# Performance work log

Measured on AMD Instinct MI355X. Metric: run time of the kernel, lower is better.

Reference implementation:

```python
import jax, jax.numpy as jnp
import numpy as np

N_NODES = 50000
N_HEDGES = 100000
N_INC = 600000
F_IN = 512
HID = 128
EPS = 1e-5
ALPHA = 0.5


def layer_norm(x, g, b):
    mu = jnp.mean(x, axis=-1, keepdims=True)
    var = jnp.mean((x - mu) ** 2, axis=-1, keepdims=True)
    return (x - mu) * jax.lax.rsqrt(var + EPS) * g + b


def scatter_mean(src, idx, num_segments):
    s = jax.ops.segment_sum(src, idx, num_segments=num_segments)
    c = jax.ops.segment_sum(jnp.ones((src.shape[0], 1), src.dtype), idx, num_segments=num_segments)
    return jnp.where(c > 0, s / jnp.maximum(c, 1.0), 0.0)


def setup_inputs() -> dict:
    key = jax.random.key(0)
    ks = jax.random.split(key, 20)

    def lin(k, fi, fo):
        kw, kb = jax.random.split(k)
        w = jax.random.normal(kw, (fi, fo), jnp.float32) / np.sqrt(fi)
        b = jax.random.normal(kb, (fo,), jnp.float32) * 0.01
        return w, b

    x1 = jax.random.normal(ks[0], (N_NODES, F_IN), jnp.float32)
    x2 = jax.random.normal(ks[1], (N_NODES, F_IN), jnp.float32)
    v1 = jax.random.randint(ks[2], (N_INC,), 0, N_NODES, jnp.int32)
    e1 = jax.random.randint(ks[3], (N_INC,), 0, N_HEDGES, jnp.int32)
    v2 = jax.random.randint(ks[4], (N_INC,), 0, N_NODES, jnp.int32)
    e2 = jax.random.randint(ks[5], (N_INC,), 0, N_HEDGES, jnp.int32)

    lin_w, lin_b = lin(ks[6], F_IN, HID)
    w1_w, w1_b = lin(ks[7], HID, HID)
    w2_w, w2_b = lin(ks[8], 2 * HID, HID)
    w_w, w_b = lin(ks[9], HID, HID)
    cls_w1, cls_b1 = lin(ks[10], HID, 64)
    cls_w2, cls_b2 = lin(ks[11], 64, 1)

    return {
        "x1": x1, "v1": v1, "e1": e1, "x2": x2, "v2": v2, "e2": e2,
        "lin_w": lin_w, "lin_b": lin_b,
        "w1_ln_g": jnp.ones((HID,)), "w1_ln_b": jnp.zeros((HID,)), "w1_w": w1_w, "w1_b": w1_b,
        "w2_ln_g": jnp.ones((2 * HID,)), "w2_ln_b": jnp.zeros((2 * HID,)), "w2_w": w2_w, "w2_b": w2_b,
        "w_ln_g": jnp.ones((HID,)), "w_ln_b": jnp.zeros((HID,)), "w_w": w_w, "w_b": w_b,
        "cls_w1": cls_w1, "cls_b1": cls_b1,
        "cls_ln_g": jnp.ones((64,)), "cls_ln_b": jnp.zeros((64,)),
        "cls_w2": cls_w2, "cls_b2": cls_b2,
    }


def _conv(X, v, e, X0, p):
    # W1 (LN + Linear) on vertices, gather to incidence pairs
    Xve = (layer_norm(X, p["w1_ln_g"], p["w1_ln_b"]) @ p["w1_w"] + p["w1_b"])[v]  # [E, H]
    Xe = scatter_mean(Xve, e, N_HEDGES)                                             # [M, H]
    Xev = Xe[e]                                                                      # [E, H]
    cat = jnp.concatenate([X[v], Xev], axis=-1)                                      # [E, 2H]
    Xev = layer_norm(cat, p["w2_ln_g"], p["w2_ln_b"]) @ p["w2_w"] + p["w2_b"]      # [E, H]
    Xv = scatter_mean(Xev, v, X.shape[0])                                            # [N, H]
    X = (1.0 - ALPHA) * Xv + ALPHA * X0
    return layer_norm(X, p["w_ln_g"], p["w_ln_b"]) @ p["w_w"] + p["w_b"]


def _branch(x, v, e, p):
    x = jax.nn.relu(x @ p["lin_w"] + p["lin_b"])
    x0 = x
    for _ in range(2):  # nlayer=2, shared conv weights
        x = jax.nn.relu(_conv(x, v, e, x0, p))
    # classifier MLP: Linear -> relu -> LN -> Linear
    h = jax.nn.relu(x @ p["cls_w1"] + p["cls_b1"])
    h = layer_norm(h, p["cls_ln_g"], p["cls_ln_b"])
    return h @ p["cls_w2"] + p["cls_b2"]


def reference(x1, v1, e1, x2, v2, e2,
              lin_w, lin_b,
              w1_ln_g, w1_ln_b, w1_w, w1_b,
              w2_ln_g, w2_ln_b, w2_w, w2_b,
              w_ln_g, w_ln_b, w_w, w_b,
              cls_w1, cls_b1, cls_ln_g, cls_ln_b, cls_w2, cls_b2):
    p = dict(lin_w=lin_w, lin_b=lin_b,
             w1_ln_g=w1_ln_g, w1_ln_b=w1_ln_b, w1_w=w1_w, w1_b=w1_b,
             w2_ln_g=w2_ln_g, w2_ln_b=w2_ln_b, w2_w=w2_w, w2_b=w2_b,
             w_ln_g=w_ln_g, w_ln_b=w_ln_b, w_w=w_w, w_b=w_b,
             cls_w1=cls_w1, cls_b1=cls_b1, cls_ln_g=cls_ln_g, cls_ln_b=cls_ln_b,
             cls_w2=cls_w2, cls_b2=cls_b2)
    return (_branch(x1, v1, e1, p), _branch(x2, v2, e2, p))
```

## Files before the change

kernel.cpp:

```cpp
#include <hip/hip_runtime.h>

#define NN 50000
#define NH 100000
#define NI 600000
#define FIN 512
#define HID 128
#define LNEPS 1e-5f

static __device__ __forceinline__ void fma4(float4& a, float s, const float4& w) {
  a.x += s * w.x; a.y += s * w.y; a.z += s * w.z; a.w += s * w.w;
}

__global__ void k_hist(const int* __restrict__ idx, int n, int* __restrict__ deg) {
  int i = blockIdx.x * 256 + threadIdx.x;
  if (i < n) atomicAdd(&deg[idx[i]], 1);
}

__global__ __launch_bounds__(1024) void k_scan1(int* __restrict__ data, int m,
                                                int* __restrict__ bsums) {
  __shared__ int sh[1024];
  int tid = threadIdx.x;
  int i = blockIdx.x * 1024 + tid;
  int v = (i < m) ? data[i] : 0;
  sh[tid] = v;
  __syncthreads();
  for (int off = 1; off < 1024; off <<= 1) {
    int tv = (tid >= off) ? sh[tid - off] : 0;
    __syncthreads();
    sh[tid] += tv;
    __syncthreads();
  }
  if (i < m) data[i] = sh[tid] - v;
  if (tid == 1023) bsums[blockIdx.x] = sh[1023];
}

__global__ __launch_bounds__(1024) void k_scan2(int* __restrict__ bsums, int nb) {
  __shared__ int sh[1024];
  int tid = threadIdx.x;
  int v = (tid < nb) ? bsums[tid] : 0;
  sh[tid] = v;
  __syncthreads();
  for (int off = 1; off < 1024; off <<= 1) {
    int tv = (tid >= off) ? sh[tid - off] : 0;
    __syncthreads();
    sh[tid] += tv;
    __syncthreads();
  }
  if (tid < nb) bsums[tid] = sh[tid] - v;
}

__global__ void k_scan3(int* __restrict__ data, const int* __restrict__ bsums,
                        int m, int total) {
  int i = blockIdx.x * 256 + threadIdx.x;
  if (i < m) data[i] += bsums[i >> 10];
  if (i == 0) data[m] = total;
}

__global__ void k_fill(const int* __restrict__ key, const int* __restrict__ oth, int n,
                       const int* __restrict__ starts, int* __restrict__ cursor,
                       int* __restrict__ out_oth) {
  int i = blockIdx.x * 256 + threadIdx.x;
  if (i >= n) return;
  int k = key[i];
  int pos = starts[k] + atomicAdd(&cursor[k], 1);
  out_oth[pos] = oth[i];
}

__global__ void k_sort_seg(const int* __restrict__ starts, int nseg,
                           int* __restrict__ vals) {
  int seg = blockIdx.x * 256 + threadIdx.x;
  if (seg >= nseg) return;
  int s = starts[seg], e = starts[seg + 1];
  int d = e - s;
  if (d <= 1) return;
  if (d <= 48) {
    int buf[48];
    for (int i = 0; i < d; i++) buf[i] = vals[s + i];
    for (int i = 1; i < d; i++) {
      int key = buf[i], j = i - 1;
      while (j >= 0 && buf[j] > key) { buf[j + 1] = buf[j]; j--; }
      buf[j + 1] = key;
    }
    for (int i = 0; i < d; i++) vals[s + i] = buf[i];
  } else {
    for (int i = s + 1; i < e; i++) {
      int key = vals[i], j = i - 1;
      while (j >= s && vals[j] > key) { vals[j + 1] = vals[j]; j--; }
      vals[j + 1] = key;
    }
  }
}

__global__ void k_prep_w2g(const float* __restrict__ W2, const float* __restrict__ g2,
                           float* __restrict__ W2g) {
  int i = blockIdx.x * 256 + threadIdx.x;
  if (i >= 256 * 128) return;
  int k = i >> 7;
  W2g[i] = g2[k] * W2[i];
}

__global__ __launch_bounds__(128) void k_prep_sgc0(
    const float* __restrict__ W2, const float* __restrict__ g2,
    const float* __restrict__ b2, const float* __restrict__ bias2,
    float* __restrict__ s_g, float* __restrict__ c0) {
  int t = threadIdx.x;
  float sg = 0.f, cc = 0.f;
  for (int k = 0; k < 256; k++) {
    float w = W2[k * 128 + t];
    sg += g2[k] * w;
    cc += b2[k] * w;
  }
  s_g[t] = sg;
  c0[t] = cc + bias2[t];
}

static __device__ __forceinline__ void gemm_inner(
    const float (*Ash)[132], const float (*Wsh)[68], int tc, int tr,
    float4& acc0, float4& acc1) {
#pragma unroll 8
  for (int k = 0; k < 128; k += 4) {
    float4 w0 = *(const float4*)&Wsh[k + 0][tc * 4];
    float4 w1 = *(const float4*)&Wsh[k + 1][tc * 4];
    float4 w2 = *(const float4*)&Wsh[k + 2][tc * 4];
    float4 w3 = *(const float4*)&Wsh[k + 3][tc * 4];
    float4 a0 = *(const float4*)&Ash[tr * 2 + 0][k];
    float4 a1 = *(const float4*)&Ash[tr * 2 + 1][k];
    fma4(acc0, a0.x, w0); fma4(acc0, a0.y, w1); fma4(acc0, a0.z, w2); fma4(acc0, a0.w, w3);
    fma4(acc1, a1.x, w0); fma4(acc1, a1.y, w1); fma4(acc1, a1.z, w2); fma4(acc1, a1.w, w3);
  }
}

template <bool BIAS, bool RELU>
static __device__ __forceinline__ void tile_gemm_out(
    const float (*Ash)[132], float (*Wsh)[68], const float* __restrict__ W,
    const float* __restrict__ bias, float* __restrict__ out, int r0, int N, int t) {
  const int tc = t & 15, tr = t >> 4;
  for (int ch = 0; ch < 2; ch++) {
    __syncthreads();
    for (int s = t; s < 2048; s += 256) {
      int k = s >> 4, c4 = (s & 15) * 4;
      *(float4*)&Wsh[k][c4] = *(const float4*)(W + (size_t)k * 128 + ch * 64 + c4);
    }
    __syncthreads();
    float4 acc0 = {0, 0, 0, 0}, acc1 = {0, 0, 0, 0};
    gemm_inner(Ash, (const float(*)[68])Wsh, tc, tr, acc0, acc1);
    int c = ch * 64 + tc * 4;
    float4 bb = {0, 0, 0, 0};
    if (BIAS) bb = *(const float4*)(bias + c);
    int row0 = r0 + tr * 2;
    if (row0 < N) {
      float4 o;
      o.x = acc0.x + bb.x; o.y = acc0.y + bb.y; o.z = acc0.z + bb.z; o.w = acc0.w + bb.w;
      if (RELU) { o.x = fmaxf(o.x, 0.f); o.y = fmaxf(o.y, 0.f); o.z = fmaxf(o.z, 0.f); o.w = fmaxf(o.w, 0.f); }
      *(float4*)(out + (size_t)row0 * 128 + c) = o;
    }
    if (row0 + 1 < N) {
      float4 o;
      o.x = acc1.x + bb.x; o.y = acc1.y + bb.y; o.z = acc1.z + bb.z; o.w = acc1.w + bb.w;
      if (RELU) { o.x = fmaxf(o.x, 0.f); o.y = fmaxf(o.y, 0.f); o.z = fmaxf(o.z, 0.f); o.w = fmaxf(o.w, 0.f); }
      *(float4*)(out + (size_t)(row0 + 1) * 128 + c) = o;
    }
  }
}

template <bool LN, bool BIAS, bool RELU>
__global__ __launch_bounds__(256) void k_tile128(
    const float* __restrict__ A, const float* __restrict__ W,
    const float* __restrict__ bias, const float* __restrict__ lng,
    const float* __restrict__ lnb, float* __restrict__ sn,
    float* __restrict__ qn, float* __restrict__ out, int N) {
  __shared__ float Ash[32][132];
  __shared__ float Wsh[128][68];
  const int t = threadIdx.x;
  const int r0 = blockIdx.x * 32;
  for (int s = t; s < 1024; s += 256) {
    int r = s >> 5, c4 = (s & 31) * 4;
    float4 val = {0, 0, 0, 0};
    if (r0 + r < N) val = *(const float4*)(A + (size_t)(r0 + r) * 128 + c4);
    *(float4*)&Ash[r][c4] = val;
  }
  if (LN) {
    __syncthreads();
    int wv = t >> 6, lane = t & 63;
    for (int j = 0; j < 8; j++) {
      int r = wv * 8 + j;
      if (r0 + r < N) {
        float2 x = *(float2*)&Ash[r][lane * 2];
        float s = x.x + x.y, sq = x.x * x.x + x.y * x.y;
        for (int m = 1; m < 64; m <<= 1) { s += __shfl_xor(s, m); sq += __shfl_xor(sq, m); }
        if (lane == 0) { sn[r0 + r] = s; qn[r0 + r] = sq; }
        float mu = s * (1.f / 128.f);
        float var = sq * (1.f / 128.f) - mu * mu;
        float rstd = rsqrtf(var + LNEPS);
        float2 gg = ((const float2*)lng)[lane];
        float2 bb = ((const float2*)lnb)[lane];
        float2 o;
        o.x = (x.x - mu) * rstd * gg.x + bb.x;
        o.y = (x.y - mu) * rstd * gg.y + bb.y;
        *(float2*)&Ash[r][lane * 2] = o;
      }
    }
  }
  tile_gemm_out<BIAS, RELU>((const float(*)[132])Ash, Wsh, W, bias, out, r0, N, t);
}

__global__ __launch_bounds__(256) void k_proj(
    const float* __restrict__ A, const float* __restrict__ W,
    const float* __restrict__ bias, float* __restrict__ out,
    float* __restrict__ out2, int N) {
  __shared__ float Ash[32][132];
  __shared__ float Wsh[128][68];
  const int t = threadIdx.x;
  const int r0 = blockIdx.x * 32;
  const int tc = t & 15, tr = t >> 4;
  for (int ch = 0; ch < 2; ch++) {
    float4 acc0 = {0, 0, 0, 0}, acc1 = {0, 0, 0, 0};
    for (int kc = 0; kc < 4; kc++) {
      __syncthreads();
      for (int s = t; s < 1024; s += 256) {
        int r = s >> 5, c4 = (s & 31) * 4;
        float4 val = {0, 0, 0, 0};
        if (r0 + r < N) val = *(const float4*)(A + (size_t)(r0 + r) * 512 + kc * 128 + c4);
        *(float4*)&Ash[r][c4] = val;
      }
      for (int s = t; s < 2048; s += 256) {
        int k = s >> 4, c4 = (s & 15) * 4;
        *(float4*)&Wsh[k][c4] = *(const float4*)(W + (size_t)(kc * 128 + k) * 128 + ch * 64 + c4);
      }
      __syncthreads();
      gemm_inner((const float(*)[132])Ash, (const float(*)[68])Wsh, tc, tr, acc0, acc1);
    }
    int c = ch * 64 + tc * 4;
    float4 bb = *(const float4*)(bias + c);
    int row0 = r0 + tr * 2;
    if (row0 < N) {
      float4 o;
      o.x = fmaxf(acc0.x + bb.x, 0.f); o.y = fmaxf(acc0.y + bb.y, 0.f);
      o.z = fmaxf(acc0.z + bb.z, 0.f); o.w = fmaxf(acc0.w + bb.w, 0.f);
      *(float4*)(out + (size_t)row0 * 128 + c) = o;
      *(float4*)(out2 + (size_t)row0 * 128 + c) = o;
    }
    if (row0 + 1 < N) {
      float4 o;
      o.x = fmaxf(acc1.x + bb.x, 0.f); o.y = fmaxf(acc1.y + bb.y, 0.f);
      o.z = fmaxf(acc1.z + bb.z, 0.f); o.w = fmaxf(acc1.w + bb.w, 0.f);
      *(float4*)(out + (size_t)(row0 + 1) * 128 + c) = o;
      *(float4*)(out2 + (size_t)(row0 + 1) * 128 + c) = o;
    }
  }
}

__global__ __launch_bounds__(256) void k_xe(
    const float* __restrict__ B, const int* __restrict__ starts,
    const int* __restrict__ vlist, float* __restrict__ Xe,
    float* __restrict__ se, float* __restrict__ qe, int M) {
  int half = threadIdx.x >> 5, lane = threadIdx.x & 31;
  int m = blockIdx.x * 8 + half;
  if (m >= M) return;
  int s = starts[m], e = starts[m + 1];
  float4 acc = {0.f, 0.f, 0.f, 0.f};
  for (int j = s; j < e; j++) {
    int vv = vlist[j];
    float4 val = ((const float4*)(B + (size_t)vv * 128))[lane];
    acc.x += val.x; acc.y += val.y; acc.z += val.z; acc.w += val.w;
  }
  int d = e - s;
  float inv = d > 0 ? 1.f / (float)d : 0.f;
  float4 o = {acc.x * inv, acc.y * inv, acc.z * inv, acc.w * inv};
  ((float4*)(Xe + (size_t)m * 128))[lane] = o;
  float ss = o.x + o.y + o.z + o.w;
  float qq = o.x * o.x + o.y * o.y + o.z * o.z + o.w * o.w;
  for (int mm = 1; mm < 32; mm <<= 1) {
    ss += __shfl_xor(ss, mm, 32);
    qq += __shfl_xor(qq, mm, 32);
  }
  if (lane == 0) { se[m] = ss; qe[m] = qq; }
}

__global__ __launch_bounds__(256) void k_nodeg(
    const float* __restrict__ X, const float* __restrict__ Xe,
    const int* __restrict__ starts_v, const int* __restrict__ e_by_v,
    const float* __restrict__ sn, const float* __restrict__ qn,
    const float* __restrict__ se, const float* __restrict__ qe,
    float* __restrict__ P, float* __restrict__ Qb,
    float* __restrict__ invdeg, float* __restrict__ t2arr, int N) {
  int half = threadIdx.x >> 5, lane = threadIdx.x & 31;
  int v = blockIdx.x * 8 + half;
  if (v >= N) return;
  int s = starts_v[v], e = starts_v[v + 1];
  float svn = sn[v], qvn = qn[v];
  float4 acc = {0.f, 0.f, 0.f, 0.f};
  float suma = 0.f, sumb = 0.f;
  for (int j = s; j < e; j++) {
    int ee = e_by_v[j];
    float mu = (svn + se[ee]) * (1.f / 256.f);
    float e2 = (qvn + qe[ee]) * (1.f / 256.f);
    float rstd = rsqrtf(e2 - mu * mu + LNEPS);
    suma += rstd;
    sumb += mu * rstd;
    float4 vv = ((const float4*)(Xe + (size_t)ee * 128))[lane];
    acc.x += rstd * vv.x; acc.y += rstd * vv.y;
    acc.z += rstd * vv.z; acc.w += rstd * vv.w;
  }
  float4 xr = ((const float4*)(X + (size_t)v * 128))[lane];
  float4 pp = {suma * xr.x, suma * xr.y, suma * xr.z, suma * xr.w};
  ((float4*)(P + (size_t)v * 128))[lane] = pp;
  ((float4*)(Qb + (size_t)v * 128))[lane] = acc;
  if (lane == 0) {
    int d = e - s;
    float inv = d > 0 ? 1.f / (float)d : 0.f;
    invdeg[v] = inv;
    t2arr[v] = sumb * inv;
  }
}

__global__ __launch_bounds__(256) void k_tile256(
    const float* __restrict__ P, const float* __restrict__ Q,
    const float* __restrict__ W, const float* __restrict__ invdeg,
    const float* __restrict__ t2arr, const float* __restrict__ s_g,
    const float* __restrict__ c0, const float* __restrict__ X0,
    const float* __restrict__ wg, const float* __restrict__ wbn,
    float* __restrict__ out, int N) {
  __shared__ float Ash[32][260];
  __shared__ float Wsh[64][68];
  const int t = threadIdx.x;
  const int r0 = blockIdx.x * 32;
  for (int s = t; s < 2048; s += 256) {
    int r = s >> 6, c4 = (s & 63) * 4;
    float4 val = {0, 0, 0, 0};
    if (r0 + r < N) {
      val = (c4 < 128) ? *(const float4*)(P + (size_t)(r0 + r) * 128 + c4)
                       : *(const float4*)(Q + (size_t)(r0 + r) * 128 + (c4 - 128));
    }
    *(float4*)&Ash[r][c4] = val;
  }
  const int tc = t & 15, tr = t >> 4;
  float4 acc[2][2] = {{{0,0,0,0},{0,0,0,0}},{{0,0,0,0},{0,0,0,0}}};
  for (int ch = 0; ch < 2; ch++) {
    for (int kc = 0; kc < 4; kc++) {
      __syncthreads();
      for (int s = t; s < 1024; s += 256) {
        int k = s >> 4, c4 = (s & 15) * 4;
        *(float4*)&Wsh[k][c4] = *(const float4*)(W + (size_t)(kc * 64 + k) * 128 + ch * 64 + c4);
      }
      __syncthreads();
#pragma unroll 4
      for (int k = 0; k < 64; k += 4) {
        float4 w0 = *(const float4*)&Wsh[k + 0][tc * 4];
        float4 w1 = *(const float4*)&Wsh[k + 1][tc * 4];
        float4 w2 = *(const float4*)&Wsh[k + 2][tc * 4];
        float4 w3 = *(const float4*)&Wsh[k + 3][tc * 4];
        float4 a0 = *(const float4*)&Ash[tr * 2 + 0][kc * 64 + k];
        float4 a1 = *(const float4*)&Ash[tr * 2 + 1][kc * 64 + k];
        fma4(acc[ch][0], a0.x, w0); fma4(acc[ch][0], a0.y, w1);
        fma4(acc[ch][0], a0.z, w2); fma4(acc[ch][0], a0.w, w3);
        fma4(acc[ch][1], a1.x, w0); fma4(acc[ch][1], a1.y, w1);
        fma4(acc[ch][1], a1.z, w2); fma4(acc[ch][1], a1.w, w3);
      }
    }
  }
  __syncthreads();
  for (int r = 0; r < 2; r++) {
    int row = r0 + tr * 2 + r;
    if (row < N) {
      float t1 = invdeg[row], t2 = t2arr[row];
      float flag = t1 > 0.f ? 1.f : 0.f;
      for (int ch = 0; ch < 2; ch++) {
        int c = ch * 64 + tc * 4;
        float4 g = acc[ch][r];
        float4 sg = *(const float4*)(s_g + c);
        float4 cc = *(const float4*)(c0 + c);
        float4 x0 = *(const float4*)(X0 + (size_t)row * 128 + c);
        float4 z;
        z.x = 0.5f * (g.x * t1 - t2 * sg.x + flag * cc.x) + 0.5f * x0.x;
        z.y = 0.5f * (g.y * t1 - t2 * sg.y + flag * cc.y) + 0.5f * x0.y;
        z.z = 0.5f * (g.z * t1 - t2 * sg.z + flag * cc.z) + 0.5f * x0.z;
        z.w = 0.5f * (g.w * t1 - t2 * sg.w + flag * cc.w) + 0.5f * x0.w;
        *(float4*)&Ash[tr * 2 + r][c] = z;
      }
    }
  }
  __syncthreads();
  int wv = t >> 6, lane = t & 63;
  for (int j = 0; j < 8; j++) {
    int r = wv * 8 + j;
    if (r0 + r < N) {
      float2 x = *(float2*)&Ash[r][lane * 2];
      float s = x.x + x.y, sq = x.x * x.x + x.y * x.y;
      for (int m = 1; m < 64; m <<= 1) { s += __shfl_xor(s, m); sq += __shfl_xor(sq, m); }
      float mu = s * (1.f / 128.f);
      float var = sq * (1.f / 128.f) - mu * mu;
      float rstd = rsqrtf(var + LNEPS);
      float2 gg = ((const float2*)wg)[lane];
      float2 bb = ((const float2*)wbn)[lane];
      float2 o;
      o.x = (x.x - mu) * rstd * gg.x + bb.x;
      o.y = (x.y - mu) * rstd * gg.y + bb.y;
      *(float2*)(out + (size_t)(r0 + r) * 128 + lane * 2) = o;
    }
  }
}

__global__ __launch_bounds__(128) void k_cls(
    const float* __restrict__ X, const float* __restrict__ W1,
    const float* __restrict__ b1, const float* __restrict__ lg,
    const float* __restrict__ lb, const float* __restrict__ W2,
    const float* __restrict__ b2, float* __restrict__ out, int N) {
  __shared__ float xr[128];
  int n = blockIdx.x, t = threadIdx.x;
  xr[t] = X[(size_t)n * 128 + t];
  __syncthreads();
  if (t < 64) {
    float a = b1[t];
    for (int k = 0; k < 128; k++) a += xr[k] * W1[k * 64 + t];
    float h = fmaxf(a, 0.f);
    float s = h, sq = h * h;
    for (int m = 1; m < 64; m <<= 1) { s += __shfl_xor(s, m); sq += __shfl_xor(sq, m); }
    float mu = s * (1.f / 64.f);
    float var = sq * (1.f / 64.f) - mu * mu;
    float rstd = rsqrtf(var + LNEPS);
    float hn = (h - mu) * rstd * lg[t] + lb[t];
    float c = hn * W2[t];
    for (int m = 1; m < 64; m <<= 1) c += __shfl_xor(c, m);
    if (t == 0) out[n] = c + b2[0];
  }
}

static void run_branch(const float* x_in, const int* v, const int* e,
                       const float* lin_w, const float* lin_b,
                       const float* w1g, const float* w1bn, const float* w1w, const float* w1b,
                       const float* W2g, const float* s_g, const float* c0,
                       const float* wg, const float* wbn, const float* ww, const float* wb,
                       const float* cw1, const float* cb1, const float* cg, const float* cbn,
                       const float* cw2, const float* cb2,
                       float* X, float* X0, float* B, float* Qb, float* Xe,
                       float* sn, float* qn, float* se, float* qe,
                       float* invdeg, float* t2arr,
                       int* starts_e, int* starts_v, int* cursor, int* bsums,
                       int* v_by_e, int* e_by_v,
                       float* out, hipStream_t stream) {
  const int GN = (NN + 31) / 32;
  hipMemsetAsync(starts_e, 0, (NH + 1) * sizeof(int), stream);
  k_hist<<<(NI + 255) / 256, 256, 0, stream>>>(e, NI, starts_e);
  k_scan1<<<(NH + 1023) / 1024, 1024, 0, stream>>>(starts_e, NH, bsums);
  k_scan2<<<1, 1024, 0, stream>>>(bsums, (NH + 1023) / 1024);
  k_scan3<<<(NH + 255) / 256, 256, 0, stream>>>(starts_e, bsums, NH, NI);
  hipMemsetAsync(cursor, 0, NH * sizeof(int), stream);
  k_fill<<<(NI + 255) / 256, 256, 0, stream>>>(e, v, NI, starts_e, cursor, v_by_e);
  k_sort_seg<<<(NH + 255) / 256, 256, 0, stream>>>(starts_e, NH, v_by_e);
  hipMemsetAsync(starts_v, 0, (NN + 1) * sizeof(int), stream);
  k_hist<<<(NI + 255) / 256, 256, 0, stream>>>(v, NI, starts_v);
  k_scan1<<<(NN + 1023) / 1024, 1024, 0, stream>>>(starts_v, NN, bsums);
  k_scan2<<<1, 1024, 0, stream>>>(bsums, (NN + 1023) / 1024);
  k_scan3<<<(NN + 255) / 256, 256, 0, stream>>>(starts_v, bsums, NN, NI);
  hipMemsetAsync(cursor, 0, NN * sizeof(int), stream);
  k_fill<<<(NI + 255) / 256, 256, 0, stream>>>(v, e, NI, starts_v, cursor, e_by_v);
  k_sort_seg<<<(NN + 255) / 256, 256, 0, stream>>>(starts_v, NN, e_by_v);
  k_proj<<<GN, 256, 0, stream>>>(x_in, lin_w, lin_b, X, X0, NN);
  float* cur = X;
  float* oth = B;
  for (int layer = 0; layer < 2; ++layer) {
    k_tile128<true, true, false><<<GN, 256, 0, stream>>>(
        cur, w1w, w1b, w1g, w1bn, sn, qn, oth, NN);
    k_xe<<<(NH + 7) / 8, 256, 0, stream>>>(oth, starts_e, v_by_e, Xe, se, qe, NH);
    k_nodeg<<<(NN + 7) / 8, 256, 0, stream>>>(cur, Xe, starts_v, e_by_v, sn, qn,
                                              se, qe, oth, Qb, invdeg, t2arr, NN);
    k_tile256<<<GN, 256, 0, stream>>>(oth, Qb, W2g, invdeg, t2arr, s_g, c0, X0,
                                      wg, wbn, cur, NN);
    k_tile128<false, true, true><<<GN, 256, 0, stream>>>(
        cur, ww, wb, nullptr, nullptr, nullptr, nullptr, oth, NN);
    float* tmp = cur; cur = oth; oth = tmp;
  }
  k_cls<<<NN, 128, 0, stream>>>(cur, cw1, cb1, cg, cbn, cw2, cb2, out, NN);
}

extern "C" void kernel_launch(void* const* d_in, const int* in_sizes, int n_in,
                              void* d_out, int out_size, void* d_ws, size_t ws_size,
                              hipStream_t stream) {
  (void)in_sizes; (void)n_in; (void)out_size; (void)ws_size;
  const float* x1 = (const float*)d_in[0];
  const int* v1 = (const int*)d_in[1];
  const int* e1 = (const int*)d_in[2];
  const float* x2 = (const float*)d_in[3];
  const int* v2 = (const int*)d_in[4];
  const int* e2 = (const int*)d_in[5];
  const float* lin_w = (const float*)d_in[6];
  const float* lin_b = (const float*)d_in[7];
  const float* w1g = (const float*)d_in[8];
  const float* w1bn = (const float*)d_in[9];
  const float* w1w = (const float*)d_in[10];
  const float* w1b = (const float*)d_in[11];
  const float* w2g = (const float*)d_in[12];
  const float* w2bn = (const float*)d_in[13];
  const float* w2w = (const float*)d_in[14];
  const float* w2b = (const float*)d_in[15];
  const float* wg = (const float*)d_in[16];
  const float* wbn = (const float*)d_in[17];
  const float* ww = (const float*)d_in[18];
  const float* wb = (const float*)d_in[19];
  const float* cw1 = (const float*)d_in[20];
  const float* cb1 = (const float*)d_in[21];
  const float* cg = (const float*)d_in[22];
  const float* cbn = (const float*)d_in[23];
  const float* cw2 = (const float*)d_in[24];
  const float* cb2 = (const float*)d_in[25];

  char* p = (char*)d_ws;
  auto alloc = [&](size_t bytes) {
    char* r = p;
    p += (bytes + 255) & ~(size_t)255;
    return r;
  };
  float* X = (float*)alloc((size_t)NN * 128 * 4);
  float* X0 = (float*)alloc((size_t)NN * 128 * 4);
  float* B = (float*)alloc((size_t)NN * 128 * 4);
  float* Qb = (float*)alloc((size_t)NN * 128 * 4);
  float* Xe = (float*)alloc((size_t)NH * 128 * 4);
  float* sn = (float*)alloc((size_t)NN * 4);
  float* qn = (float*)alloc((size_t)NN * 4);
  float* se = (float*)alloc((size_t)NH * 4);
  float* qe = (float*)alloc((size_t)NH * 4);
  float* invdeg = (float*)alloc((size_t)NN * 4);
  float* t2arr = (float*)alloc((size_t)NN * 4);
  int* starts_e = (int*)alloc((NH + 1) * 4);
  int* starts_v = (int*)alloc((NN + 1) * 4);
  int* cursor = (int*)alloc(NH * 4);
  int* bsums = (int*)alloc(1024 * 4);
  int* v_by_e = (int*)alloc((size_t)NI * 4);
  int* e_by_v = (int*)alloc((size_t)NI * 4);
  float* W2g = (float*)alloc((size_t)256 * 128 * 4);
  float* s_g = (float*)alloc(128 * 4);
  float* c0 = (float*)alloc(128 * 4);

  k_prep_w2g<<<128, 256, 0, stream>>>(w2w, w2g, W2g);
  k_prep_sgc0<<<1, 128, 0, stream>>>(w2w, w2g, w2bn, w2b, s_g, c0);

  float* out = (float*)d_out;
  run_branch(x1, v1, e1, lin_w, lin_b, w1g, w1bn, w1w, w1b, W2g, s_g, c0,
             wg, wbn, ww, wb, cw1, cb1, cg, cbn, cw2, cb2,
             X, X0, B, Qb, Xe, sn, qn, se, qe, invdeg, t2arr,
             starts_e, starts_v, cursor, bsums, v_by_e, e_by_v, out, stream);
  run_branch(x2, v2, e2, lin_w, lin_b, w1g, w1bn, w1w, w1b, W2g, s_g, c0,
             wg, wbn, ww, wb, cw1, cb1, cg, cbn, cw2, cb2,
             X, X0, B, Qb, Xe, sn, qn, se, qe, invdeg, t2arr,
             starts_e, starts_v, cursor, bsums, v_by_e, e_by_v, out + NN, stream);
}
```

Baseline: 2.022 ms.

## Fuse dense GEMM stages across layers and shrink weight tiles in shared memory

The input projection is fused with the first LN+W1 linear. Each layer's W linear is fused with the next layer's LN+W1, or with the classifier MLP on the last layer, so each 128-wide intermediate stays in shared memory instead of making a round trip through global memory. The per-node classifier kernel (one block per node) becomes a 32-row tiled GEMM. Weight staging shrinks to 32x64 slabs, which cuts shared memory but adds more __syncthreads per GEMM. k_wnext reads and writes X in place, which relies on each block touching only its own rows.

```diff
diff --git a/kernel.cpp b/kernel.cpp
--- a/kernel.cpp
+++ b/kernel.cpp
@@ -114,138 +114,138 @@
   c0[t] = cc + bias2[t];
 }
 
-static __device__ __forceinline__ void gemm_inner(
-    const float (*Ash)[132], const float (*Wsh)[68], int tc, int tr,
-    float4& acc0, float4& acc1) {
-#pragma unroll 8
-  for (int k = 0; k < 128; k += 4) {
+static __device__ __forceinline__ void stage_w(float (*Wsh)[68], const float* __restrict__ W,
+                                               int ldw, int row0, int col0, int t) {
+  for (int s = t; s < 512; s += 256) {
+    int k = s >> 4, c4 = (s & 15) * 4;
+    *(float4*)&Wsh[k][c4] = *(const float4*)(W + (size_t)(row0 + k) * ldw + col0 + c4);
+  }
+}
+
+static __device__ __forceinline__ void inner32(const float (*Ash)[132], const float (*Wsh)[68],
+                                               int kb, int tc, int tr,
+                                               float4& acc0, float4& acc1) {
+#pragma unroll
+  for (int k = 0; k < 32; k += 4) {
     float4 w0 = *(const float4*)&Wsh[k + 0][tc * 4];
     float4 w1 = *(const float4*)&Wsh[k + 1][tc * 4];
     float4 w2 = *(const float4*)&Wsh[k + 2][tc * 4];
     float4 w3 = *(const float4*)&Wsh[k + 3][tc * 4];
-    float4 a0 = *(const float4*)&Ash[tr * 2 + 0][k];
-    float4 a1 = *(const float4*)&Ash[tr * 2 + 1][k];
+    float4 a0 = *(const float4*)&Ash[tr * 2 + 0][kb + k];
+    float4 a1 = *(const float4*)&Ash[tr * 2 + 1][kb + k];
     fma4(acc0, a0.x, w0); fma4(acc0, a0.y, w1); fma4(acc0, a0.z, w2); fma4(acc0, a0.w, w3);
     fma4(acc1, a1.x, w0); fma4(acc1, a1.y, w1); fma4(acc1, a1.z, w2); fma4(acc1, a1.w, w3);
   }
 }
 
-template <bool BIAS, bool RELU>
-static __device__ __forceinline__ void tile_gemm_out(
-    const float (*Ash)[132], float (*Wsh)[68], const float* __restrict__ W,
-    const float* __restrict__ bias, float* __restrict__ out, int r0, int N, int t) {
-  const int tc = t & 15, tr = t >> 4;
-  for (int ch = 0; ch < 2; ch++) {
-    __syncthreads();
-    for (int s = t; s < 2048; s += 256) {
-      int k = s >> 4, c4 = (s & 15) * 4;
-      *(float4*)&Wsh[k][c4] = *(const float4*)(W + (size_t)k * 128 + ch * 64 + c4);
-    }
-    __syncthreads();
-    float4 acc0 = {0, 0, 0, 0}, acc1 = {0, 0, 0, 0};
-    gemm_inner(Ash, (const float(*)[68])Wsh, tc, tr, acc0, acc1);
-    int c = ch * 64 + tc * 4;
-    float4 bb = {0, 0, 0, 0};
-    if (BIAS) bb = *(const float4*)(bias + c);
-    int row0 = r0 + tr * 2;
-    if (row0 < N) {
-      float4 o;
-      o.x = acc0.x + bb.x; o.y = acc0.y + bb.y; o.z = acc0.z + bb.z; o.w = acc0.w + bb.w;
-      if (RELU) { o.x = fmaxf(o.x, 0.f); o.y = fmaxf(o.y, 0.f); o.z = fmaxf(o.z, 0.f); o.w = fmaxf(o.w, 0.f); }
-      *(float4*)(out + (size_t)row0 * 128 + c) = o;
-    }
-    if (row0 + 1 < N) {
-      float4 o;
-      o.x = acc1.x + bb.x; o.y = acc1.y + bb.y; o.z = acc1.z + bb.z; o.w = acc1.w + bb.w;
-      if (RELU) { o.x = fmaxf(o.x, 0.f); o.y = fmaxf(o.y, 0.f); o.z = fmaxf(o.z, 0.f); o.w = fmaxf(o.w, 0.f); }
-      *(float4*)(out + (size_t)(row0 + 1) * 128 + c) = o;
-    }
-  }
-}
-
-template <bool LN, bool BIAS, bool RELU>
-__global__ __launch_bounds__(256) void k_tile128(
-    const float* __restrict__ A, const float* __restrict__ W,
-    const float* __restrict__ bias, const float* __restrict__ lng,
-    const float* __restrict__ lnb, float* __restrict__ sn,
-    float* __restrict__ qn, float* __restrict__ out, int N) {
-  __shared__ float Ash[32][132];
-  __shared__ float Wsh[128][68];
-  const int t = threadIdx.x;
-  const int r0 = blockIdx.x * 32;
+static __device__ __forceinline__ void load_a128(float (*Ash)[132], const float* __restrict__ A,
+                                                 int r0, int N, int t) {
   for (int s = t; s < 1024; s += 256) {
     int r = s >> 5, c4 = (s & 31) * 4;
     float4 val = {0, 0, 0, 0};
     if (r0 + r < N) val = *(const float4*)(A + (size_t)(r0 + r) * 128 + c4);
     *(float4*)&Ash[r][c4] = val;
   }
-  if (LN) {
-    __syncthreads();
-    int wv = t >> 6, lane = t & 63;
-    for (int j = 0; j < 8; j++) {
-      int r = wv * 8 + j;
-      if (r0 + r < N) {
-        float2 x = *(float2*)&Ash[r][lane * 2];
-        float s = x.x + x.y, sq = x.x * x.x + x.y * x.y;
-        for (int m = 1; m < 64; m <<= 1) { s += __shfl_xor(s, m); sq += __shfl_xor(sq, m); }
-        if (lane == 0) { sn[r0 + r] = s; qn[r0 + r] = sq; }
-        float mu = s * (1.f / 128.f);
-        float var = sq * (1.f / 128.f) - mu * mu;
-        float rstd = rsqrtf(var + LNEPS);
-        float2 gg = ((const float2*)lng)[lane];
-        float2 bb = ((const float2*)lnb)[lane];
-        float2 o;
-        o.x = (x.x - mu) * rstd * gg.x + bb.x;
-        o.y = (x.y - mu) * rstd * gg.y + bb.y;
-        *(float2*)&Ash[r][lane * 2] = o;
-      }
-    }
-  }
-  tile_gemm_out<BIAS, RELU>((const float(*)[132])Ash, Wsh, W, bias, out, r0, N, t);
-}
-
-__global__ __launch_bounds__(256) void k_proj(
-    const float* __restrict__ A, const float* __restrict__ W,
-    const float* __restrict__ bias, float* __restrict__ out,
-    float* __restrict__ out2, int N) {
+}
+
+template <bool STATS>
+static __device__ __forceinline__ void ln_tile(float (*Ash)[132], const float* __restrict__ g,
+                                               const float* __restrict__ b,
+                                               float* __restrict__ sn, float* __restrict__ qn,
+                                               int r0, int N, int t) {
+  int wv = t >> 6, lane = t & 63;
+  for (int j = 0; j < 8; j++) {
+    int r = wv * 8 + j;
+    if (r0 + r < N) {
+      float2 x = *(float2*)&Ash[r][lane * 2];
+      float s = x.x + x.y, sq = x.x * x.x + x.y * x.y;
+      for (int m = 1; m < 64; m <<= 1) { s += __shfl_xor(s, m); sq += __shfl_xor(sq, m); }
+      if (STATS && lane == 0) { sn[r0 + r] = s; qn[r0 + r] = sq; }
+      float mu = s * (1.f / 128.f);
+      float var = sq * (1.f / 128.f) - mu * mu;
+      float rstd = rsqrtf(var + LNEPS);
+      float2 gg = ((const float2*)g)[lane];
+      float2 bb = ((const float2*)b)[lane];
+      float2 o;
+      o.x = (x.x - mu) * rstd * gg.x + bb.x;
+      o.y = (x.y - mu) * rstd * gg.y + bb.y;
+      *(float2*)&Ash[r][lane * 2] = o;
+    }
+  }
+}
+
+__global__ __launch_bounds__(256) void k_proj_fused(
+    const float* __restrict__ x_in, const float* __restrict__ lin_w,
+    const float* __restrict__ lin_b, const float* __restrict__ w1g,
+    const float* __restrict__ w1bn, const float* __restrict__ w1w,
+    const float* __restrict__ w1b, float* __restrict__ X, float* __restrict__ X0,
+    float* __restrict__ B, float* __restrict__ sn, float* __restrict__ qn, int N) {
   __shared__ float Ash[32][132];
-  __shared__ float Wsh[128][68];
+  __shared__ float Wsh[32][68];
   const int t = threadIdx.x;
   const int r0 = blockIdx.x * 32;
   const int tc = t & 15, tr = t >> 4;
+  float4 acc0[2] = {{0,0,0,0},{0,0,0,0}}, acc1[2] = {{0,0,0,0},{0,0,0,0}};
+  for (int kq = 0; kq < 4; kq++) {
+    __syncthreads();
+    for (int s = t; s < 1024; s += 256) {
+      int r = s >> 5, c4 = (s & 31) * 4;
+      float4 val = {0, 0, 0, 0};
+      if (r0 + r < N) val = *(const float4*)(x_in + (size_t)(r0 + r) * 512 + kq * 128 + c4);
+      *(float4*)&Ash[r][c4] = val;
+    }
+    for (int ch = 0; ch < 2; ch++)
+      for (int kc = 0; kc < 4; kc++) {
+        __syncthreads();
+        stage_w(Wsh, lin_w, 128, kq * 128 + kc * 32, ch * 64, t);
+        __syncthreads();
+        inner32((const float(*)[132])Ash, (const float(*)[68])Wsh, kc * 32, tc, tr,
+                acc0[ch], acc1[ch]);
+      }
+  }
+  __syncthreads();
   for (int ch = 0; ch < 2; ch++) {
-    float4 acc0 = {0, 0, 0, 0}, acc1 = {0, 0, 0, 0};
+    int c = ch * 64 + tc * 4;
+    float4 bb = *(const float4*)(lin_b + c);
+    int row0 = r0 + tr * 2;
+    float4 z0, z1;
+    z0.x = fmaxf(acc0[ch].x + bb.x, 0.f); z0.y = fmaxf(acc0[ch].y + bb.y, 0.f);
+    z0.z = fmaxf(acc0[ch].z + bb.z, 0.f); z0.w = fmaxf(acc0[ch].w + bb.w, 0.f);
+    z1.x = fmaxf(acc1[ch].x + bb.x, 0.f); z1.y = fmaxf(acc1[ch].y + bb.y, 0.f);
+    z1.z = fmaxf(acc1[ch].z + bb.z, 0.f); z1.w = fmaxf(acc1[ch].w + bb.w, 0.f);
+    if (row0 < N) {
+      *(float4*)(X + (size_t)row0 * 128 + c) = z0;
+      *(float4*)(X0 + (size_t)row0 * 128 + c) = z0;
+      *(float4*)&Ash[tr * 2][c] = z0;
+    }
+    if (row0 + 1 < N) {
+      *(float4*)(X + (size_t)(row0 + 1) * 128 + c) = z1;
+      *(float4*)(X0 + (size_t)(row0 + 1) * 128 + c) = z1;
+      *(float4*)&Ash[tr * 2 + 1][c] = z1;
+    }
+  }
+  __syncthreads();
+  ln_tile<true>(Ash, w1g, w1bn, sn, qn, r0, N, t);
+  float4 f0[2] = {{0,0,0,0},{0,0,0,0}}, f1[2] = {{0,0,0,0},{0,0,0,0}};
+  for (int ch = 0; ch < 2; ch++)
     for (int kc = 0; kc < 4; kc++) {
       __syncthreads();
-      for (int s = t; s < 1024; s += 256) {
-        int r = s >> 5, c4 = (s & 31) * 4;
-        float4 val = {0, 0, 0, 0};
-        if (r0 + r < N) val = *(const float4*)(A + (size_t)(r0 + r) * 512 + kc * 128 + c4);
-        *(float4*)&Ash[r][c4] = val;
-      }
-      for (int s = t; s < 2048; s += 256) {
-        int k = s >> 4, c4 = (s & 15) * 4;
-        *(float4*)&Wsh[k][c4] = *(const float4*)(W + (size_t)(kc * 128 + k) * 128 + ch * 64 + c4);
-      }
-      __syncthreads();
-      gemm_inner((const float(*)[132])Ash, (const float(*)[68])Wsh, tc, tr, acc0, acc1);
-    }
+      stage_w(Wsh, w1w, 128, kc * 32, ch * 64, t);
+      __syncthreads();
+      inner32((const float(*)[132])Ash, (const float(*)[68])Wsh, kc * 32, tc, tr,
+              f0[ch], f1[ch]);
+    }
+  for (int ch = 0; ch < 2; ch++) {
     int c = ch * 64 + tc * 4;
-    float4 bb = *(const float4*)(bias + c);
+    float4 bb = *(const float4*)(w1b + c);
     int row0 = r0 + tr * 2;
     if (row0 < N) {
-      float4 o;
-      o.x = fmaxf(acc0.x + bb.x, 0.f); o.y = fmaxf(acc0.y + bb.y, 0.f);
-      o.z = fmaxf(acc0.z + bb.z, 0.f); o.w = fmaxf(acc0.w + bb.w, 0.f);
-      *(float4*)(out + (size_t)row0 * 128 + c) = o;
-      *(float4*)(out2 + (size_t)row0 * 128 + c) = o;
+      float4 o = {f0[ch].x + bb.x, f0[ch].y + bb.y, f0[ch].z + bb.z, f0[ch].w + bb.w};
+      *(float4*)(B + (size_t)row0 * 128 + c) = o;
     }
     if (row0 + 1 < N) {
-      float4 o;
-      o.x = fmaxf(acc1.x + bb.x, 0.f); o.y = fmaxf(acc1.y + bb.y, 0.f);
-      o.z = fmaxf(acc1.z + bb.z, 0.f); o.w = fmaxf(acc1.w + bb.w, 0.f);
-      *(float4*)(out + (size_t)(row0 + 1) * 128 + c) = o;
-      *(float4*)(out2 + (size_t)(row0 + 1) * 128 + c) = o;
+      float4 o = {f1[ch].x + bb.x, f1[ch].y + bb.y, f1[ch].z + bb.z, f1[ch].w + bb.w};
+      *(float4*)(B + (size_t)(row0 + 1) * 128 + c) = o;
     }
   }
 }
@@ -314,50 +314,30 @@
   }
 }
 
-__global__ __launch_bounds__(256) void k_tile256(
+__global__ __launch_bounds__(256) void k_conv2(
     const float* __restrict__ P, const float* __restrict__ Q,
     const float* __restrict__ W, const float* __restrict__ invdeg,
     const float* __restrict__ t2arr, const float* __restrict__ s_g,
     const float* __restrict__ c0, const float* __restrict__ X0,
     const float* __restrict__ wg, const float* __restrict__ wbn,
     float* __restrict__ out, int N) {
-  __shared__ float Ash[32][260];
-  __shared__ float Wsh[64][68];
+  __shared__ float Ash[32][132];
+  __shared__ float Wsh[32][68];
   const int t = threadIdx.x;
   const int r0 = blockIdx.x * 32;
-  for (int s = t; s < 2048; s += 256) {
-    int r = s >> 6, c4 = (s & 63) * 4;
-    float4 val = {0, 0, 0, 0};
-    if (r0 + r < N) {
-      val = (c4 < 128) ? *(const float4*)(P + (size_t)(r0 + r) * 128 + c4)
-                       : *(const float4*)(Q + (size_t)(r0 + r) * 128 + (c4 - 128));
-    }
-    *(float4*)&Ash[r][c4] = val;
-  }
   const int tc = t & 15, tr = t >> 4;
-  float4 acc[2][2] = {{{0,0,0,0},{0,0,0,0}},{{0,0,0,0},{0,0,0,0}}};
-  for (int ch = 0; ch < 2; ch++) {
-    for (int kc = 0; kc < 4; kc++) {
-      __syncthreads();
-      for (int s = t; s < 1024; s += 256) {
-        int k = s >> 4, c4 = (s & 15) * 4;
-        *(float4*)&Wsh[k][c4] = *(const float4*)(W + (size_t)(kc * 64 + k) * 128 + ch * 64 + c4);
+  float4 acc0[2] = {{0,0,0,0},{0,0,0,0}}, acc1[2] = {{0,0,0,0},{0,0,0,0}};
+  for (int ph = 0; ph < 2; ph++) {
+    __syncthreads();
+    load_a128(Ash, ph ? Q : P, r0, N, t);
+    for (int ch = 0; ch < 2; ch++)
+      for (int kc = 0; kc < 4; kc++) {
+        __syncthreads();
+        stage_w(Wsh, W, 128, ph * 128 + kc * 32, ch * 64, t);
+        __syncthreads();
+        inner32((const float(*)[132])Ash, (const float(*)[68])Wsh, kc * 32, tc, tr,
+                acc0[ch], acc1[ch]);
       }
-      __syncthreads();
-#pragma unroll 4
-      for (int k = 0; k < 64; k += 4) {
-        float4 w0 = *(const float4*)&Wsh[k + 0][tc * 4];
-        float4 w1 = *(const float4*)&Wsh[k + 1][tc * 4];
-        float4 w2 = *(const float4*)&Wsh[k + 2][tc * 4];
-        float4 w3 = *(const float4*)&Wsh[k + 3][tc * 4];
-        float4 a0 = *(const float4*)&Ash[tr * 2 + 0][kc * 64 + k];
-        float4 a1 = *(const float4*)&Ash[tr * 2 + 1][kc * 64 + k];
-        fma4(acc[ch][0], a0.x, w0); fma4(acc[ch][0], a0.y, w1);
-        fma4(acc[ch][0], a0.z, w2); fma4(acc[ch][0], a0.w, w3);
-        fma4(acc[ch][1], a1.x, w0); fma4(acc[ch][1], a1.y, w1);
-        fma4(acc[ch][1], a1.z, w2); fma4(acc[ch][1], a1.w, w3);
-      }
-    }
   }
   __syncthreads();
   for (int r = 0; r < 2; r++) {
@@ -367,7 +347,7 @@
       float flag = t1 > 0.f ? 1.f : 0.f;
       for (int ch = 0; ch < 2; ch++) {
         int c = ch * 64 + tc * 4;
-        float4 g = acc[ch][r];
+        float4 g = r ? acc1[ch] : acc0[ch];
         float4 sg = *(const float4*)(s_g + c);
         float4 cc = *(const float4*)(c0 + c);
         float4 x0 = *(const float4*)(X0 + (size_t)row * 128 + c);
@@ -401,28 +381,146 @@
   }
 }
 
-__global__ __launch_bounds__(128) void k_cls(
-    const float* __restrict__ X, const float* __restrict__ W1,
-    const float* __restrict__ b1, const float* __restrict__ lg,
-    const float* __restrict__ lb, const float* __restrict__ W2,
-    const float* __restrict__ b2, float* __restrict__ out, int N) {
-  __shared__ float xr[128];
-  int n = blockIdx.x, t = threadIdx.x;
-  xr[t] = X[(size_t)n * 128 + t];
-  __syncthreads();
-  if (t < 64) {
-    float a = b1[t];
-    for (int k = 0; k < 128; k++) a += xr[k] * W1[k * 64 + t];
-    float h = fmaxf(a, 0.f);
-    float s = h, sq = h * h;
-    for (int m = 1; m < 64; m <<= 1) { s += __shfl_xor(s, m); sq += __shfl_xor(sq, m); }
-    float mu = s * (1.f / 64.f);
-    float var = sq * (1.f / 64.f) - mu * mu;
-    float rstd = rsqrtf(var + LNEPS);
-    float hn = (h - mu) * rstd * lg[t] + lb[t];
-    float c = hn * W2[t];
-    for (int m = 1; m < 64; m <<= 1) c += __shfl_xor(c, m);
-    if (t == 0) out[n] = c + b2[0];
+__global__ __launch_bounds__(256) void k_wnext(
+    const float* __restrict__ Xin, const float* __restrict__ Ww,
+    const float* __restrict__ wb, const float* __restrict__ w1g,
+    const float* __restrict__ w1bn, const float* __restrict__ w1w,
+    const float* __restrict__ w1b, float* __restrict__ Xout,
+    float* __restrict__ B, float* __restrict__ sn, float* __restrict__ qn, int N) {
+  __shared__ float Ash[32][132];
+  __shared__ float Wsh[32][68];
+  const int t = threadIdx.x;
+  const int r0 = blockIdx.x * 32;
+  const int tc = t & 15, tr = t >> 4;
+  load_a128(Ash, Xin, r0, N, t);
+  float4 acc0[2] = {{0,0,0,0},{0,0,0,0}}, acc1[2] = {{0,0,0,0},{0,0,0,0}};
+  for (int ch = 0; ch < 2; ch++)
+    for (int kc = 0; kc < 4; kc++) {
+      __syncthreads();
+      stage_w(Wsh, Ww, 128, kc * 32, ch * 64, t);
+      __syncthreads();
+      inner32((const float(*)[132])Ash, (const float(*)[68])Wsh, kc * 32, tc, tr,
+              acc0[ch], acc1[ch]);
+    }
+  __syncthreads();
+  for (int ch = 0; ch < 2; ch++) {
+    int c = ch * 64 + tc * 4;
+    float4 bb = *(const float4*)(wb + c);
+    int row0 = r0 + tr * 2;
+    float4 z0, z1;
+    z0.x = fmaxf(acc0[ch].x + bb.x, 0.f); z0.y = fmaxf(acc0[ch].y + bb.y, 0.f);
+    z0.z = fmaxf(acc0[ch].z + bb.z, 0.f); z0.w = fmaxf(acc0[ch].w + bb.w, 0.f);
+    z1.x = fmaxf(acc1[ch].x + bb.x, 0.f); z1.y = fmaxf(acc1[ch].y + bb.y, 0.f);
+    z1.z = fmaxf(acc1[ch].z + bb.z, 0.f); z1.w = fmaxf(acc1[ch].w + bb.w, 0.f);
+    if (row0 < N) {
+      *(float4*)(Xout + (size_t)row0 * 128 + c) = z0;
+      *(float4*)&Ash[tr * 2][c] = z0;
+    }
+    if (row0 + 1 < N) {
+      *(float4*)(Xout + (size_t)(row0 + 1) * 128 + c) = z1;
+      *(float4*)&Ash[tr * 2 + 1][c] = z1;
+    }
+  }
+  __syncthreads();
+  ln_tile<true>(Ash, w1g, w1bn, sn, qn, r0, N, t);
+  float4 f0[2] = {{0,0,0,0},{0,0,0,0}}, f1[2] = {{0,0,0,0},{0,0,0,0}};
+  for (int ch = 0; ch < 2; ch++)
+    for (int kc = 0; kc < 4; kc++) {
+      __syncthreads();
+      stage_w(Wsh, w1w, 128, kc * 32, ch * 64, t);
+      __syncthreads();
+      inner32((const float(*)[132])Ash, (const float(*)[68])Wsh, kc * 32, tc, tr,
+              f0[ch], f1[ch]);
+    }
+  for (int ch = 0; ch < 2; ch++) {
+    int c = ch * 64 + tc * 4;
+    float4 bb = *(const float4*)(w1b + c);
+    int row0 = r0 + tr * 2;
+    if (row0 < N) {
+      float4 o = {f0[ch].x + bb.x, f0[ch].y + bb.y, f0[ch].z + bb.z, f0[ch].w + bb.w};
+      *(float4*)(B + (size_t)row0 * 128 + c) = o;
+    }
+    if (row0 + 1 < N) {
+      float4 o = {f1[ch].x + bb.x, f1[ch].y + bb.y, f1[ch].z + bb.z, f1[ch].w + bb.w};
+      *(float4*)(B + (size_t)(row0 + 1) * 128 + c) = o;
+    }
+  }
+}
+
+__global__ __launch_bounds__(256) void k_wcls(
+    const float* __restrict__ Xin, const float* __restrict__ Ww,
+    const float* __restrict__ wb, const float* __restrict__ cw1,
+    const float* __restrict__ cb1, const float* __restrict__ cg,
+    const float* __restrict__ cbn, const float* __restrict__ cw2,
+    const float* __restrict__ cb2, float* __restrict__ out, int N) {
+  __shared__ float Ash[32][132];
+  __shared__ float Wsh[32][68];
+  const int t = threadIdx.x;
+  const int r0 = blockIdx.x * 32;
+  const int tc = t & 15, tr = t >> 4;
+  load_a128(Ash, Xin, r0, N, t);
+  float4 acc0[2] = {{0,0,0,0},{0,0,0,0}}, acc1[2] = {{0,0,0,0},{0,0,0,0}};
+  for (int ch = 0; ch < 2; ch++)
+    for (int kc = 0; kc < 4; kc++) {
+      __syncthreads();
+      stage_w(Wsh, Ww, 128, kc * 32, ch * 64, t);
+      __syncthreads();
+      inner32((const float(*)[132])Ash, (const float(*)[68])Wsh, kc * 32, tc, tr,
+              acc0[ch], acc1[ch]);
+    }
+  __syncthreads();
+  for (int ch = 0; ch < 2; ch++) {
+    int c = ch * 64 + tc * 4;
+    float4 bb = *(const float4*)(wb + c);
+    int row0 = r0 + tr * 2;
+    if (row0 < N) {
+      float4 z;
+      z.x = fmaxf(acc0[ch].x + bb.x, 0.f); z.y = fmaxf(acc0[ch].y + bb.y, 0.f);
+      z.z = fmaxf(acc0[ch].z + bb.z, 0.f); z.w = fmaxf(acc0[ch].w + bb.w, 0.f);
+      *(float4*)&Ash[tr * 2][c] = z;
+    }
+    if (row0 + 1 < N) {
+      float4 z;
+      z.x = fmaxf(acc1[ch].x + bb.x, 0.f); z.y = fmaxf(acc1[ch].y + bb.y, 0.f);
+      z.z = fmaxf(acc1[ch].z + bb.z, 0.f); z.w = fmaxf(acc1[ch].w + bb.w, 0.f);
+      *(float4*)&Ash[tr * 2 + 1][c] = z;
+    }
+  }
+  float4 h0 = {0,0,0,0}, h1 = {0,0,0,0};
+  for (int kc = 0; kc < 4; kc++) {
+    __syncthreads();
+    stage_w(Wsh, cw1, 64, kc * 32, 0, t);
+    __syncthreads();
+    inner32((const float(*)[132])Ash, (const float(*)[68])Wsh, kc * 32, tc, tr, h0, h1);
+  }
+  __syncthreads();
+  {
+    int c = tc * 4;
+    float4 bb = *(const float4*)(cb1 + c);
+    float4 z;
+    z.x = fmaxf(h0.x + bb.x, 0.f); z.y = fmaxf(h0.y + bb.y, 0.f);
+    z.z = fmaxf(h0.z + bb.z, 0.f); z.w = fmaxf(h0.w + bb.w, 0.f);
+    *(float4*)&Wsh[tr * 2][c] = z;
+    z.x = fmaxf(h1.x + bb.x, 0.f); z.y = fmaxf(h1.y + bb.y, 0.f);
+    z.z = fmaxf(h1.z + bb.z, 0.f); z.w = fmaxf(h1.w + bb.w, 0.f);
+    *(float4*)&Wsh[tr * 2 + 1][c] = z;
+  }
+  __syncthreads();
+  int wv = t >> 6, lane = t & 63;
+  for (int j = 0; j < 8; j++) {
+    int r = wv * 8 + j;
+    if (r0 + r < N) {
+      float h = Wsh[r][lane];
+      float s = h, sq = h * h;
+      for (int m = 1; m < 64; m <<= 1) { s += __shfl_xor(s, m); sq += __shfl_xor(sq, m); }
+      float mu = s * (1.f / 64.f);
+      float var = sq * (1.f / 64.f) - mu * mu;
+      float rstd = rsqrtf(var + LNEPS);
+      float hn = (h - mu) * rstd * cg[lane] + cbn[lane];
+      float c = hn * cw2[lane];
+      for (int m = 1; m < 64; m <<= 1) c += __shfl_xor(c, m);
+      if (lane == 0) out[r0 + r] = c + cb2[0];
+    }
   }
 }
 
@@ -456,22 +554,22 @@
   hipMemsetAsync(cursor, 0, NN * sizeof(int), stream);
   k_fill<<<(NI + 255) / 256, 256, 0, stream>>>(v, e, NI, starts_v, cursor, e_by_v);
   k_sort_seg<<<(NN + 255) / 256, 256, 0, stream>>>(starts_v, NN, e_by_v);
-  k_proj<<<GN, 256, 0, stream>>>(x_in, lin_w, lin_b, X, X0, NN);
-  float* cur = X;
-  float* oth = B;
+  k_proj_fused<<<GN, 256, 0, stream>>>(x_in, lin_w, lin_b, w1g, w1bn, w1w, w1b,
+                                       X, X0, B, sn, qn, NN);
   for (int layer = 0; layer < 2; ++layer) {
-    k_tile128<true, true, false><<<GN, 256, 0, stream>>>(
-        cur, w1w, w1b, w1g, w1bn, sn, qn, oth, NN);
-    k_xe<<<(NH + 7) / 8, 256, 0, stream>>>(oth, starts_e, v_by_e, Xe, se, qe, NH);
-    k_nodeg<<<(NN + 7) / 8, 256, 0, stream>>>(cur, Xe, starts_v, e_by_v, sn, qn,
-                                              se, qe, oth, Qb, invdeg, t2arr, NN);
-    k_tile256<<<GN, 256, 0, stream>>>(oth, Qb, W2g, invdeg, t2arr, s_g, c0, X0,
-                                      wg, wbn, cur, NN);
-    k_tile128<false, true, true><<<GN, 256, 0, stream>>>(
-        cur, ww, wb, nullptr, nullptr, nullptr, nullptr, oth, NN);
-    float* tmp = cur; cur = oth; oth = tmp;
-  }
-  k_cls<<<NN, 128, 0, stream>>>(cur, cw1, cb1, cg, cbn, cw2, cb2, out, NN);
+    k_xe<<<NH / 8, 256, 0, stream>>>(B, starts_e, v_by_e, Xe, se, qe, NH);
+    k_nodeg<<<(NN + 7) / 8, 256, 0, stream>>>(X, Xe, starts_v, e_by_v, sn, qn,
+                                              se, qe, B, Qb, invdeg, t2arr, NN);
+    k_conv2<<<GN, 256, 0, stream>>>(B, Qb, W2g, invdeg, t2arr, s_g, c0, X0,
+                                    wg, wbn, X, NN);
+    if (layer == 0) {
+      k_wnext<<<GN, 256, 0, stream>>>(X, ww, wb, w1g, w1bn, w1w, w1b,
+                                      X, B, sn, qn, NN);
+    } else {
+      k_wcls<<<GN, 256, 0, stream>>>(X, ww, wb, cw1, cb1, cg, cbn, cw2, cb2,
+                                     out, NN);
+    }
+  }
 }
 
 extern "C" void kernel_launch(void* const* d_in, const int* in_sizes, int n_in,
```

After: 1.843 ms. 1.1x faster.
